# Kernel optimization log

Measured on AMD Instinct MI355X. Metric: run time of the kernel, lower is better.

## Reference

```python
import jax, jax.numpy as jnp
import numpy as np

B, N0, N1, N2 = 4, 50000, 25000, 12500
E0, E1 = 800000, 400000
CIN, CS, COUT = 32, 16, 32
EPS = 1e-5


def _xavier(k, shape):
    scale = (2.0 / (shape[0] + shape[-1])) ** 0.5
    return jax.random.normal(k, shape, jnp.float32) * scale


def setup_inputs() -> dict:
    key = jax.random.key(0)
    ks = jax.random.split(key, 32)
    inp = {
        "X": jax.random.normal(ks[0], (B, N0, CIN), jnp.float32),
        "edge_index0": jax.random.randint(ks[1], (2, E0), 0, N1),
        "edge_weight0": jax.random.uniform(ks[2], (E0,), jnp.float32),
        "res_n_id0": jax.random.randint(ks[3], (N1,), 0, N0),
        "edge_index1": jax.random.randint(ks[4], (2, E1), 0, N2),
        "edge_weight1": jax.random.uniform(ks[5], (E1,), jnp.float32),
        "res_n_id1": jax.random.randint(ks[6], (N2,), 0, N1),
        # conv1 params (in=32 -> out=16, edge_channels=1)
        "Wn1": _xavier(ks[7], (CIN, CS)),
        "We1": _xavier(ks[8], (1, CS)),
        "Q1": _xavier(ks[9], (CS, CS)),
        "K1": _xavier(ks[10], (CS, CS)),
        "Watt1": _xavier(ks[11], (3 * CS, 1)),
        "batt1": jnp.zeros((1,), jnp.float32),
        "Wc1": _xavier(ks[12], (2 * CS, CS)),
        "bc1": jnp.zeros((CS,), jnp.float32),
        # conv2 params (in=16 -> out=32, edge_channels=1)
        "Wn2": _xavier(ks[13], (CS, COUT)),
        "We2": _xavier(ks[14], (1, COUT)),
        "Q2": _xavier(ks[15], (COUT, COUT)),
        "K2": _xavier(ks[16], (COUT, COUT)),
        "Watt2": _xavier(ks[17], (3 * COUT, 1)),
        "batt2": jnp.zeros((1,), jnp.float32),
        "Wc2": _xavier(ks[18], (2 * COUT, COUT)),
        "bc2": jnp.zeros((COUT,), jnp.float32),
    }
    return inp


def egnn_conv(x_src, x_dst, edge_index, edge_feature, num_dst,
              Wn, We, Q, K, Watt, batt, Wc, bc):
    # x_src: [B, Nsrc, Cin], x_dst: [B, Ndst, Cin], edge_feature: [E, 1]
    xs = jnp.matmul(x_src, Wn)        # [B, Nsrc, C]
    xd = jnp.matmul(x_dst, Wn)        # [B, Ndst, C]
    edge_emb = jnp.matmul(edge_feature, We)  # [E, C]

    src, dst = edge_index[0], edge_index[1]
    x_j = xs[:, src]                  # gather [B, E, C]
    x_i = xd[:, dst]                  # gather [B, E, C]

    query = jnp.matmul(x_j, Q)        # [B, E, C]
    key = jnp.matmul(x_i, K)          # [B, E, C]
    ee = jnp.broadcast_to(edge_emb[None], query.shape)  # [B, E, C]
    att_feature = jnp.concatenate([query, key, ee], axis=-1)  # [B, E, 3C]
    att = jax.nn.sigmoid(jnp.matmul(att_feature, Watt) + batt)  # [B, E, 1]
    gate = jax.nn.sigmoid(edge_emb)[None]  # [1, E, C]
    msg = att * x_j * gate            # [B, E, C]

    # scatter-add over destination nodes
    aggr = jnp.zeros((msg.shape[0], num_dst, msg.shape[-1]), msg.dtype)
    aggr = aggr.at[:, dst].add(msg)   # [B, Ndst, C]

    out = jnp.matmul(jnp.concatenate([xd, aggr], axis=-1), Wc) + bc  # [B, Ndst, C]
    mean = jnp.mean(out, axis=(0, 2), keepdims=True)
    var = jnp.var(out, axis=(0, 2), keepdims=True, ddof=1)  # torch var is unbiased
    out = (out - mean) / jnp.sqrt(var + EPS)
    return xd + out


def reference(X, edge_index0, edge_weight0, res_n_id0,
              edge_index1, edge_weight1, res_n_id1,
              Wn1, We1, Q1, K1, Watt1, batt1, Wc1, bc1,
              Wn2, We2, Q2, K2, Watt2, batt2, Wc2, bc2):
    h = egnn_conv(X, X[:, res_n_id0], edge_index0, edge_weight0[:, None], N1,
                  Wn1, We1, Q1, K1, Watt1, batt1, Wc1, bc1)
    h = jax.nn.leaky_relu(h, 0.01)
    h = egnn_conv(h, h[:, res_n_id1], edge_index1, edge_weight1[:, None], N2,
                  Wn2, We2, Q2, K2, Watt2, batt2, Wc2, bc2)
    h = jax.nn.leaky_relu(h, 0.01)
    return h
```

## Files before the change

### kernel.cpp

```cpp
#include <hip/hip_runtime.h>

#define B_ 4
#define N0_ 50000
#define N1_ 25000
#define N2_ 12500
#define E0_ 800000
#define E1_ 400000
#define CIN_ 32
#define CS_ 16
#define COUT_ 32
#define EPS_ 1e-5f
#define CAP_ 80
#define SST1_ 3200
#define SST2_ 1600

__device__ __forceinline__ int slice_of(int d) { return (d >> 2) & 7; }
__device__ __forceinline__ int curix(int d, int sst) {
    return ((d >> 2) & 7) * sst + ((d >> 5) << 2) + (d & 3);
}
__device__ __forceinline__ float sigmoidf_(float x) {
    return __builtin_amdgcn_rcpf(1.0f + __expf(-x));
}

__global__ void prep_kernel(const float* __restrict__ Q1, const float* __restrict__ K1,
                            const float* __restrict__ Watt1,
                            const float* __restrict__ Q2, const float* __restrict__ K2,
                            const float* __restrict__ Watt2,
                            const float* __restrict__ We1, const float* __restrict__ We2,
                            float* __restrict__ qv1, float* __restrict__ kv1,
                            float* __restrict__ qv2, float* __restrict__ kv2,
                            float* __restrict__ se) {
    int t = threadIdx.x;
    if (t < CS_) {
        float q = 0.f, k = 0.f;
        for (int c = 0; c < CS_; ++c) {
            q += Q1[t * CS_ + c] * Watt1[c];
            k += K1[t * CS_ + c] * Watt1[CS_ + c];
        }
        qv1[t] = q; kv1[t] = k;
    }
    if (t < COUT_) {
        float q = 0.f, k = 0.f;
        for (int c = 0; c < COUT_; ++c) {
            q += Q2[t * COUT_ + c] * Watt2[c];
            k += K2[t * COUT_ + c] * Watt2[COUT_ + c];
        }
        qv2[t] = q; kv2[t] = k;
    }
    if (t == 0) {
        float s1 = 0.f, s2 = 0.f;
        for (int c = 0; c < CS_; ++c) s1 += We1[c] * Watt1[2 * CS_ + c];
        for (int c = 0; c < COUT_; ++c) s2 += We2[c] * Watt2[2 * COUT_ + c];
        se[0] = s1; se[1] = s2;
    }
}

__global__ void node_xform1(const float* __restrict__ X, const int* __restrict__ res,
                            const float* __restrict__ Wn,
                            const float* __restrict__ qv, const float* __restrict__ kv,
                            unsigned short* __restrict__ xsb, float* __restrict__ xd_t,
                            float* __restrict__ aj, float* __restrict__ ai) {
    int lane = threadIdx.x & 63;
    int n = blockIdx.x * (blockDim.x >> 6) + (threadIdx.x >> 6);
    if (n >= N1_) return;
    int b = lane >> 4;
    int c = lane & 15;
    int rn = res[n];
    const float4* Xs4 = (const float4*)(X + ((size_t)b * N0_ + n) * CIN_);
    const float4* Xd4 = (const float4*)(X + ((size_t)b * N0_ + rn) * CIN_);
    float s = 0.f, d = 0.f;
#pragma unroll
    for (int k4 = 0; k4 < CIN_ / 4; ++k4) {
        float4 xs4 = Xs4[k4];
        float4 xd4 = Xd4[k4];
        int k = 4 * k4;
        float w0 = Wn[(k + 0) * CS_ + c], w1 = Wn[(k + 1) * CS_ + c];
        float w2 = Wn[(k + 2) * CS_ + c], w3 = Wn[(k + 3) * CS_ + c];
        s += xs4.x * w0 + xs4.y * w1 + xs4.z * w2 + xs4.w * w3;
        d += xd4.x * w0 + xd4.y * w1 + xd4.z * w2 + xd4.w * w3;
    }
    xsb[(size_t)n * 64 + lane] = (unsigned short)((__float_as_uint(s) + 0x8000u) >> 16);
    xd_t[(size_t)n * 64 + lane] = d;
    float p = s * qv[c];
    float q = d * kv[c];
#pragma unroll
    for (int m = 1; m < 16; m <<= 1) {
        p += __shfl_xor(p, m, 16);
        q += __shfl_xor(q, m, 16);
    }
    if (c == 0) {
        aj[n * 4 + b] = p;
        ai[n * 4 + b] = q;
    }
}

template <int SST>
__global__ void scatter_att(const int* __restrict__ ei, const float* __restrict__ ew,
                            int E, const float* __restrict__ aj, const float* __restrict__ ai,
                            const float* __restrict__ sep, const float* __restrict__ batt,
                            int* __restrict__ cur, uint2* __restrict__ buf) {
    int slice = blockIdx.x & 7;
    int chunk = blockIdx.x >> 3;
    int nch = gridDim.x >> 3;
    float se = sep[0], b0 = batt[0];
    for (int e = chunk * 256 + threadIdx.x; e < E; e += nch * 256) {
        int d = ei[E + e];
        if (slice_of(d) != slice) continue;
        int s = ei[e];
        float w = ew[e];
        float4 A = ((const float4*)aj)[s];
        float4 I = ((const float4*)ai)[d];
        float base = fmaf(w, se, b0);
        unsigned q =  __float2uint_rn(sigmoidf_(A.x + I.x + base) * 255.f)
                   | (__float2uint_rn(sigmoidf_(A.y + I.y + base) * 255.f) << 8)
                   | (__float2uint_rn(sigmoidf_(A.z + I.z + base) * 255.f) << 16)
                   | (__float2uint_rn(sigmoidf_(A.w + I.w + base) * 255.f) << 24);
        unsigned wv = (__float_as_uint(w) + 0x8000u) & 0xffff0000u;
        int p = atomicAdd(&cur[curix(d, SST)], 1);
        if (p < CAP_)
            buf[(size_t)d * CAP_ + p] = make_uint2(wv | (unsigned)s, q);
    }
}

__global__ void edge_fused1(const int* __restrict__ cur, const uint2* __restrict__ buf,
                            const unsigned short* __restrict__ xsb,
                            const float* __restrict__ xd_t, const float* __restrict__ We,
                            const float* __restrict__ Wc, const float* __restrict__ bc,
                            float* __restrict__ h_t) {
    int lane = threadIdx.x & 63;
    int n = blockIdx.x * (blockDim.x >> 6) + (threadIdx.x >> 6);
    if (n >= N1_) return;
    int b = lane >> 4;
    int c = lane & 15;
    int sh = 8 * b;
    float wec = We[c];
    float acc = 0.f;
    int cnt = cur[curix(n, SST1_)];
    if (cnt > CAP_) cnt = CAP_;
    const uint2* bp = buf + (size_t)n * CAP_;
    int i = 0;
    for (; i + 4 <= cnt; i += 4) {
        uint2 v0 = bp[i], v1 = bp[i + 1], v2 = bp[i + 2], v3 = bp[i + 3];
        int s0 = v0.x & 0xffff, s1 = v1.x & 0xffff;
        int s2 = v2.x & 0xffff, s3 = v3.x & 0xffff;
        float w0 = __uint_as_float(v0.x & 0xffff0000u);
        float w1 = __uint_as_float(v1.x & 0xffff0000u);
        float w2 = __uint_as_float(v2.x & 0xffff0000u);
        float w3 = __uint_as_float(v3.x & 0xffff0000u);
        float xj0 = __uint_as_float((unsigned)xsb[(size_t)s0 * 64 + lane] << 16);
        float xj1 = __uint_as_float((unsigned)xsb[(size_t)s1 * 64 + lane] << 16);
        float xj2 = __uint_as_float((unsigned)xsb[(size_t)s2 * 64 + lane] << 16);
        float xj3 = __uint_as_float((unsigned)xsb[(size_t)s3 * 64 + lane] << 16);
        float a0 = (float)((v0.y >> sh) & 0xff) * (1.f / 255.f);
        float a1 = (float)((v1.y >> sh) & 0xff) * (1.f / 255.f);
        float a2 = (float)((v2.y >> sh) & 0xff) * (1.f / 255.f);
        float a3 = (float)((v3.y >> sh) & 0xff) * (1.f / 255.f);
        acc += a0 * sigmoidf_(w0 * wec) * xj0;
        acc += a1 * sigmoidf_(w1 * wec) * xj1;
        acc += a2 * sigmoidf_(w2 * wec) * xj2;
        acc += a3 * sigmoidf_(w3 * wec) * xj3;
    }
    for (; i < cnt; ++i) {
        uint2 v0 = bp[i];
        int s0 = v0.x & 0xffff;
        float w0 = __uint_as_float(v0.x & 0xffff0000u);
        float xj0 = __uint_as_float((unsigned)xsb[(size_t)s0 * 64 + lane] << 16);
        float a0 = (float)((v0.y >> sh) & 0xff) * (1.f / 255.f);
        acc += a0 * sigmoidf_(w0 * wec) * xj0;
    }
    float xv = xd_t[(size_t)n * 64 + lane];
    float o = bc[c];
#pragma unroll
    for (int k = 0; k < CS_; ++k) {
        o += __shfl(xv, k, 16) * Wc[k * CS_ + c];
        o += __shfl(acc, k, 16) * Wc[(CS_ + k) * CS_ + c];
    }
    float s = o, sq = o * o;
#pragma unroll
    for (int m = 1; m < 64; m <<= 1) {
        s += __shfl_xor(s, m);
        sq += __shfl_xor(sq, m);
    }
    float mean = s * (1.f / 64.f);
    float var = (sq - 64.f * mean * mean) * (1.f / 63.f);
    float inv = __builtin_amdgcn_rsqf(var + EPS_);
    float v = xv + (o - mean) * inv;
    h_t[(size_t)n * 64 + lane] = v > 0.f ? v : 0.01f * v;
}

__global__ void node_xform2(const float* __restrict__ h_t, const int* __restrict__ res,
                            const float* __restrict__ Wn,
                            const float* __restrict__ qv, const float* __restrict__ kv,
                            unsigned short* __restrict__ xsb, float* __restrict__ xd_t,
                            float* __restrict__ aj, float* __restrict__ ai) {
    int lane = threadIdx.x & 63;
    int n = blockIdx.x * (blockDim.x >> 6) + (threadIdx.x >> 6);
    if (n >= N2_) return;
    int bl = lane >> 5;
    int c = lane & 31;
    int rn = res[n];
    float qc = qv[c], kc = kv[c];
#pragma unroll
    for (int j = 0; j < 2; ++j) {
        int b = bl + 2 * j;
        const float* hs = h_t + (size_t)n * 64 + b * 16;
        const float* hd = h_t + (size_t)rn * 64 + b * 16;
        float s = 0.f, d = 0.f;
#pragma unroll
        for (int k = 0; k < CS_; ++k) {
            float w = Wn[k * COUT_ + c];
            s += hs[k] * w;
            d += hd[k] * w;
        }
        xsb[(size_t)n * 128 + b * 32 + c] = (unsigned short)((__float_as_uint(s) + 0x8000u) >> 16);
        xd_t[(size_t)n * 128 + b * 32 + c] = d;
        float p = s * qc;
        float q = d * kc;
#pragma unroll
        for (int m = 1; m < 32; m <<= 1) {
            p += __shfl_xor(p, m, 32);
            q += __shfl_xor(q, m, 32);
        }
        if (c == 0) {
            aj[n * 4 + b] = p;
            ai[n * 4 + b] = q;
        }
    }
}

__global__ void edge_fused2(const int* __restrict__ cur, const uint2* __restrict__ buf,
                            const unsigned short* __restrict__ xsb,
                            const float* __restrict__ xd_t, const float* __restrict__ We,
                            const float* __restrict__ Wc, const float* __restrict__ bc,
                            float* __restrict__ out) {
    int lane = threadIdx.x & 63;
    int n = blockIdx.x * (blockDim.x >> 6) + (threadIdx.x >> 6);
    if (n >= N2_) return;
    int bl = lane >> 5;
    int c = lane & 31;
    int sh0 = 8 * bl;
    float wec = We[c];
    float acc0 = 0.f, acc1 = 0.f;
    int cnt = cur[curix(n, SST2_)];
    if (cnt > CAP_) cnt = CAP_;
    const uint2* bp = buf + (size_t)n * CAP_;
    int i = 0;
    for (; i + 4 <= cnt; i += 4) {
        uint2 v0 = bp[i], v1 = bp[i + 1], v2 = bp[i + 2], v3 = bp[i + 3];
        int s0 = v0.x & 0xffff, s1 = v1.x & 0xffff;
        int s2 = v2.x & 0xffff, s3 = v3.x & 0xffff;
        float w0 = __uint_as_float(v0.x & 0xffff0000u);
        float w1 = __uint_as_float(v1.x & 0xffff0000u);
        float w2 = __uint_as_float(v2.x & 0xffff0000u);
        float w3 = __uint_as_float(v3.x & 0xffff0000u);
        float xj00 = __uint_as_float((unsigned)xsb[(size_t)s0 * 128 + lane] << 16);
        float xj01 = __uint_as_float((unsigned)xsb[(size_t)s0 * 128 + 64 + lane] << 16);
        float xj10 = __uint_as_float((unsigned)xsb[(size_t)s1 * 128 + lane] << 16);
        float xj11 = __uint_as_float((unsigned)xsb[(size_t)s1 * 128 + 64 + lane] << 16);
        float xj20 = __uint_as_float((unsigned)xsb[(size_t)s2 * 128 + lane] << 16);
        float xj21 = __uint_as_float((unsigned)xsb[(size_t)s2 * 128 + 64 + lane] << 16);
        float xj30 = __uint_as_float((unsigned)xsb[(size_t)s3 * 128 + lane] << 16);
        float xj31 = __uint_as_float((unsigned)xsb[(size_t)s3 * 128 + 64 + lane] << 16);
        float g0 = sigmoidf_(w0 * wec);
        float g1 = sigmoidf_(w1 * wec);
        float g2 = sigmoidf_(w2 * wec);
        float g3 = sigmoidf_(w3 * wec);
        acc0 += (float)((v0.y >> sh0) & 0xff) * (1.f / 255.f) * g0 * xj00;
        acc1 += (float)((v0.y >> (sh0 + 16)) & 0xff) * (1.f / 255.f) * g0 * xj01;
        acc0 += (float)((v1.y >> sh0) & 0xff) * (1.f / 255.f) * g1 * xj10;
        acc1 += (float)((v1.y >> (sh0 + 16)) & 0xff) * (1.f / 255.f) * g1 * xj11;
        acc0 += (float)((v2.y >> sh0) & 0xff) * (1.f / 255.f) * g2 * xj20;
        acc1 += (float)((v2.y >> (sh0 + 16)) & 0xff) * (1.f / 255.f) * g2 * xj21;
        acc0 += (float)((v3.y >> sh0) & 0xff) * (1.f / 255.f) * g3 * xj30;
        acc1 += (float)((v3.y >> (sh0 + 16)) & 0xff) * (1.f / 255.f) * g3 * xj31;
    }
    for (; i < cnt; ++i) {
        uint2 v0 = bp[i];
        int s0 = v0.x & 0xffff;
        float w0 = __uint_as_float(v0.x & 0xffff0000u);
        float xj00 = __uint_as_float((unsigned)xsb[(size_t)s0 * 128 + lane] << 16);
        float xj01 = __uint_as_float((unsigned)xsb[(size_t)s0 * 128 + 64 + lane] << 16);
        float a00 = (float)((v0.y >> sh0) & 0xff) * (1.f / 255.f);
        float a01 = (float)((v0.y >> (sh0 + 16)) & 0xff) * (1.f / 255.f);
        float g0 = sigmoidf_(w0 * wec);
        acc0 += a00 * g0 * xj00;
        acc1 += a01 * g0 * xj01;
    }
    float xv0 = xd_t[(size_t)n * 128 + lane];
    float xv1 = xd_t[(size_t)n * 128 + 64 + lane];
    float o0 = bc[c], o1 = o0;
#pragma unroll
    for (int k = 0; k < COUT_; ++k) {
        float w1 = Wc[k * COUT_ + c];
        float w2 = Wc[(COUT_ + k) * COUT_ + c];
        o0 += __shfl(xv0, k, 32) * w1 + __shfl(acc0, k, 32) * w2;
        o1 += __shfl(xv1, k, 32) * w1 + __shfl(acc1, k, 32) * w2;
    }
    float s = o0 + o1, sq = o0 * o0 + o1 * o1;
#pragma unroll
    for (int m = 1; m < 64; m <<= 1) {
        s += __shfl_xor(s, m);
        sq += __shfl_xor(sq, m);
    }
    float mean = s * (1.f / 128.f);
    float var = (sq - 128.f * mean * mean) * (1.f / 127.f);
    float inv = __builtin_amdgcn_rsqf(var + EPS_);
    float v0 = xv0 + (o0 - mean) * inv;
    float v1 = xv1 + (o1 - mean) * inv;
    out[((size_t)bl * N2_ + n) * COUT_ + c] = v0 > 0.f ? v0 : 0.01f * v0;
    out[((size_t)(bl + 2) * N2_ + n) * COUT_ + c] = v1 > 0.f ? v1 : 0.01f * v1;
}

extern "C" void kernel_launch(void* const* d_in, const int* in_sizes, int n_in,
                              void* d_out, int out_size, void* d_ws, size_t ws_size,
                              hipStream_t stream) {
    (void)in_sizes; (void)n_in; (void)out_size; (void)ws_size;
    const float* X     = (const float*)d_in[0];
    const int*   ei0   = (const int*)d_in[1];
    const float* ew0   = (const float*)d_in[2];
    const int*   rn0   = (const int*)d_in[3];
    const int*   ei1   = (const int*)d_in[4];
    const float* ew1   = (const float*)d_in[5];
    const int*   rn1   = (const int*)d_in[6];
    const float* Wn1   = (const float*)d_in[7];
    const float* We1   = (const float*)d_in[8];
    const float* Q1    = (const float*)d_in[9];
    const float* K1    = (const float*)d_in[10];
    const float* Watt1 = (const float*)d_in[11];
    const float* batt1 = (const float*)d_in[12];
    const float* Wc1   = (const float*)d_in[13];
    const float* bc1   = (const float*)d_in[14];
    const float* Wn2   = (const float*)d_in[15];
    const float* We2   = (const float*)d_in[16];
    const float* Q2    = (const float*)d_in[17];
    const float* K2    = (const float*)d_in[18];
    const float* Watt2 = (const float*)d_in[19];
    const float* batt2 = (const float*)d_in[20];
    const float* Wc2   = (const float*)d_in[21];
    const float* bc2   = (const float*)d_in[22];

    const size_t BUF = (size_t)B_ * N1_ * CS_;
    float* ws  = (float*)d_ws;
    float* S0  = ws;
    float* S1  = S0 + BUF;
    unsigned short* S2 = (unsigned short*)(S1 + BUF);
    float* aj1 = (float*)(S2 + BUF);
    float* ai1 = aj1 + (size_t)N1_ * 4;
    float* aj2 = ai1 + (size_t)N1_ * 4;
    float* ai2 = aj2 + (size_t)N2_ * 4;
    uint2* ebuf = (uint2*)(ai2 + (size_t)N2_ * 4);
    int* cur1 = (int*)(ebuf + (size_t)N1_ * CAP_);
    int* cur2 = cur1 + 8 * SST1_;
    float* qv1 = (float*)(cur2 + 8 * SST2_);
    float* kv1 = qv1 + 16;
    float* qv2 = kv1 + 16;
    float* kv2 = qv2 + 32;
    float* se  = kv2 + 32;

    hipMemsetAsync(cur1, 0, (size_t)(8 * SST1_ + 8 * SST2_) * sizeof(int), stream);
    prep_kernel<<<1, 64, 0, stream>>>(Q1, K1, Watt1, Q2, K2, Watt2, We1, We2,
                                      qv1, kv1, qv2, kv2, se);

    node_xform1<<<(N1_ + 3) / 4, 256, 0, stream>>>(X, rn0, Wn1, qv1, kv1, S2, S0, aj1, ai1);
    scatter_att<SST1_><<<4096, 256, 0, stream>>>(ei0, ew0, E0_, aj1, ai1, se, batt1,
                                                 cur1, ebuf);
    edge_fused1<<<(N1_ + 3) / 4, 256, 0, stream>>>(cur1, ebuf, S2, S0, We1, Wc1, bc1, S0);

    node_xform2<<<(N2_ + 3) / 4, 256, 0, stream>>>(S0, rn1, Wn2, qv2, kv2, S2, S1, aj2, ai2);
    scatter_att<SST2_><<<2048, 256, 0, stream>>>(ei1, ew1, E1_, aj2, ai2, se + 1, batt2,
                                                 cur2, ebuf);
    edge_fused2<<<(N2_ + 3) / 4, 256, 0, stream>>>(cur2, ebuf, S2, S1, We2, Wc2, bc2,
                                                   (float*)d_out);
}
```

Baseline: 190.0 us.

## Pre-pack edge indices and weights, fold memset into prep, unroll gather by 8

A new prep kernel packs each edge's src/dst indices into one 32-bit word and its weight into a bf16 halfword, zeroes the slot counters itself instead of calling a separate memset, and still computes the attention projection vectors. The scatter kernels, which run 8 slice passes over the edge list, now read 6 bytes per edge instead of 12, cutting repeated edge-list traffic. The edge_fused1 gather loop is unrolled to 8 for more loads in flight. The packing pass adds a full read of the edge lists plus extra writes, and the 16-bit packing assumes node ids below 65536.

```diff
diff --git a/kernel.cpp b/kernel.cpp
--- a/kernel.cpp
+++ b/kernel.cpp
@@ -22,36 +22,54 @@
     return __builtin_amdgcn_rcpf(1.0f + __expf(-x));
 }
 
-__global__ void prep_kernel(const float* __restrict__ Q1, const float* __restrict__ K1,
-                            const float* __restrict__ Watt1,
-                            const float* __restrict__ Q2, const float* __restrict__ K2,
-                            const float* __restrict__ Watt2,
-                            const float* __restrict__ We1, const float* __restrict__ We2,
-                            float* __restrict__ qv1, float* __restrict__ kv1,
-                            float* __restrict__ qv2, float* __restrict__ kv2,
-                            float* __restrict__ se) {
-    int t = threadIdx.x;
-    if (t < CS_) {
-        float q = 0.f, k = 0.f;
-        for (int c = 0; c < CS_; ++c) {
-            q += Q1[t * CS_ + c] * Watt1[c];
-            k += K1[t * CS_ + c] * Watt1[CS_ + c];
-        }
-        qv1[t] = q; kv1[t] = k;
-    }
-    if (t < COUT_) {
-        float q = 0.f, k = 0.f;
-        for (int c = 0; c < COUT_; ++c) {
-            q += Q2[t * COUT_ + c] * Watt2[c];
-            k += K2[t * COUT_ + c] * Watt2[COUT_ + c];
-        }
-        qv2[t] = q; kv2[t] = k;
-    }
-    if (t == 0) {
-        float s1 = 0.f, s2 = 0.f;
-        for (int c = 0; c < CS_; ++c) s1 += We1[c] * Watt1[2 * CS_ + c];
-        for (int c = 0; c < COUT_; ++c) s2 += We2[c] * Watt2[2 * COUT_ + c];
-        se[0] = s1; se[1] = s2;
+__global__ void pack_prep(const int* __restrict__ ei0, const float* __restrict__ ew0,
+                          const int* __restrict__ ei1, const float* __restrict__ ew1,
+                          unsigned* __restrict__ pk0, unsigned short* __restrict__ wq0,
+                          unsigned* __restrict__ pk1, unsigned short* __restrict__ wq1,
+                          int* __restrict__ curz, int ztot,
+                          const float* __restrict__ Q1, const float* __restrict__ K1,
+                          const float* __restrict__ Watt1,
+                          const float* __restrict__ Q2, const float* __restrict__ K2,
+                          const float* __restrict__ Watt2,
+                          const float* __restrict__ We1, const float* __restrict__ We2,
+                          float* __restrict__ qv1, float* __restrict__ kv1,
+                          float* __restrict__ qv2, float* __restrict__ kv2,
+                          float* __restrict__ se) {
+    int gid = blockIdx.x * blockDim.x + threadIdx.x;
+    int stride = gridDim.x * blockDim.x;
+    for (int i = gid; i < ztot; i += stride) curz[i] = 0;
+    for (int e = gid; e < E0_; e += stride) {
+        pk0[e] = (unsigned)ei0[e] << 16 | (unsigned)ei0[E0_ + e];
+        wq0[e] = (unsigned short)((__float_as_uint(ew0[e]) + 0x8000u) >> 16);
+    }
+    for (int e = gid; e < E1_; e += stride) {
+        pk1[e] = (unsigned)ei1[e] << 16 | (unsigned)ei1[E1_ + e];
+        wq1[e] = (unsigned short)((__float_as_uint(ew1[e]) + 0x8000u) >> 16);
+    }
+    if (blockIdx.x == 0) {
+        int t = threadIdx.x;
+        if (t < CS_) {
+            float q = 0.f, k = 0.f;
+            for (int c = 0; c < CS_; ++c) {
+                q += Q1[t * CS_ + c] * Watt1[c];
+                k += K1[t * CS_ + c] * Watt1[CS_ + c];
+            }
+            qv1[t] = q; kv1[t] = k;
+        }
+        if (t < COUT_) {
+            float q = 0.f, k = 0.f;
+            for (int c = 0; c < COUT_; ++c) {
+                q += Q2[t * COUT_ + c] * Watt2[c];
+                k += K2[t * COUT_ + c] * Watt2[COUT_ + c];
+            }
+            qv2[t] = q; kv2[t] = k;
+        }
+        if (t == 64) {
+            float s1 = 0.f, s2 = 0.f;
+            for (int c = 0; c < CS_; ++c) s1 += We1[c] * Watt1[2 * CS_ + c];
+            for (int c = 0; c < COUT_; ++c) s2 += We2[c] * Watt2[2 * COUT_ + c];
+            se[0] = s1; se[1] = s2;
+        }
     }
 }
 
@@ -95,7 +113,7 @@
 }
 
 template <int SST>
-__global__ void scatter_att(const int* __restrict__ ei, const float* __restrict__ ew,
+__global__ void scatter_att(const unsigned* __restrict__ pk, const unsigned short* __restrict__ wq,
                             int E, const float* __restrict__ aj, const float* __restrict__ ai,
                             const float* __restrict__ sep, const float* __restrict__ batt,
                             int* __restrict__ cur, uint2* __restrict__ buf) {
@@ -104,10 +122,12 @@
     int nch = gridDim.x >> 3;
     float se = sep[0], b0 = batt[0];
     for (int e = chunk * 256 + threadIdx.x; e < E; e += nch * 256) {
-        int d = ei[E + e];
+        unsigned pv = pk[e];
+        int d = pv & 0xffff;
         if (slice_of(d) != slice) continue;
-        int s = ei[e];
-        float w = ew[e];
+        int s = pv >> 16;
+        unsigned wu = (unsigned)wq[e];
+        float w = __uint_as_float(wu << 16);
         float4 A = ((const float4*)aj)[s];
         float4 I = ((const float4*)ai)[d];
         float base = fmaf(w, se, b0);
@@ -115,10 +135,9 @@
                    | (__float2uint_rn(sigmoidf_(A.y + I.y + base) * 255.f) << 8)
                    | (__float2uint_rn(sigmoidf_(A.z + I.z + base) * 255.f) << 16)
                    | (__float2uint_rn(sigmoidf_(A.w + I.w + base) * 255.f) << 24);
-        unsigned wv = (__float_as_uint(w) + 0x8000u) & 0xffff0000u;
         int p = atomicAdd(&cur[curix(d, SST)], 1);
         if (p < CAP_)
-            buf[(size_t)d * CAP_ + p] = make_uint2(wv | (unsigned)s, q);
+            buf[(size_t)d * CAP_ + p] = make_uint2((wu << 16) | (unsigned)s, q);
     }
 }
 
@@ -139,26 +158,20 @@
     if (cnt > CAP_) cnt = CAP_;
     const uint2* bp = buf + (size_t)n * CAP_;
     int i = 0;
-    for (; i + 4 <= cnt; i += 4) {
-        uint2 v0 = bp[i], v1 = bp[i + 1], v2 = bp[i + 2], v3 = bp[i + 3];
-        int s0 = v0.x & 0xffff, s1 = v1.x & 0xffff;
-        int s2 = v2.x & 0xffff, s3 = v3.x & 0xffff;
-        float w0 = __uint_as_float(v0.x & 0xffff0000u);
-        float w1 = __uint_as_float(v1.x & 0xffff0000u);
-        float w2 = __uint_as_float(v2.x & 0xffff0000u);
-        float w3 = __uint_as_float(v3.x & 0xffff0000u);
-        float xj0 = __uint_as_float((unsigned)xsb[(size_t)s0 * 64 + lane] << 16);
-        float xj1 = __uint_as_float((unsigned)xsb[(size_t)s1 * 64 + lane] << 16);
-        float xj2 = __uint_as_float((unsigned)xsb[(size_t)s2 * 64 + lane] << 16);
-        float xj3 = __uint_as_float((unsigned)xsb[(size_t)s3 * 64 + lane] << 16);
-        float a0 = (float)((v0.y >> sh) & 0xff) * (1.f / 255.f);
-        float a1 = (float)((v1.y >> sh) & 0xff) * (1.f / 255.f);
-        float a2 = (float)((v2.y >> sh) & 0xff) * (1.f / 255.f);
-        float a3 = (float)((v3.y >> sh) & 0xff) * (1.f / 255.f);
-        acc += a0 * sigmoidf_(w0 * wec) * xj0;
-        acc += a1 * sigmoidf_(w1 * wec) * xj1;
-        acc += a2 * sigmoidf_(w2 * wec) * xj2;
-        acc += a3 * sigmoidf_(w3 * wec) * xj3;
+    for (; i + 8 <= cnt; i += 8) {
+        uint2 v[8];
+#pragma unroll
+        for (int j = 0; j < 8; ++j) v[j] = bp[i + j];
+        float xj[8], a[8], g[8];
+#pragma unroll
+        for (int j = 0; j < 8; ++j) {
+            int sj = v[j].x & 0xffff;
+            xj[j] = __uint_as_float((unsigned)xsb[(size_t)sj * 64 + lane] << 16);
+            a[j] = (float)((v[j].y >> sh) & 0xff) * (1.f / 255.f);
+            g[j] = sigmoidf_(__uint_as_float(v[j].x & 0xffff0000u) * wec);
+        }
+#pragma unroll
+        for (int j = 0; j < 8; ++j) acc += a[j] * g[j] * xj[j];
     }
     for (; i < cnt; ++i) {
         uint2 v0 = bp[i];
@@ -351,23 +364,29 @@
     uint2* ebuf = (uint2*)(ai2 + (size_t)N2_ * 4);
     int* cur1 = (int*)(ebuf + (size_t)N1_ * CAP_);
     int* cur2 = cur1 + 8 * SST1_;
-    float* qv1 = (float*)(cur2 + 8 * SST2_);
+    unsigned* pk0 = (unsigned*)(cur2 + 8 * SST2_);
+    unsigned* pk1 = pk0 + E0_;
+    unsigned short* wq0 = (unsigned short*)(pk1 + E1_);
+    unsigned short* wq1 = wq0 + E0_;
+    float* qv1 = (float*)(wq1 + E1_);
     float* kv1 = qv1 + 16;
     float* qv2 = kv1 + 16;
     float* kv2 = qv2 + 32;
     float* se  = kv2 + 32;
 
-    hipMemsetAsync(cur1, 0, (size_t)(8 * SST1_ + 8 * SST2_) * sizeof(int), stream);
-    prep_kernel<<<1, 64, 0, stream>>>(Q1, K1, Watt1, Q2, K2, Watt2, We1, We2,
-                                      qv1, kv1, qv2, kv2, se);
+    const int ztot = 8 * SST1_ + 8 * SST2_;
+    pack_prep<<<1024, 256, 0, stream>>>(ei0, ew0, ei1, ew1, pk0, wq0, pk1, wq1,
+                                        cur1, ztot,
+                                        Q1, K1, Watt1, Q2, K2, Watt2, We1, We2,
+                                        qv1, kv1, qv2, kv2, se);
 
     node_xform1<<<(N1_ + 3) / 4, 256, 0, stream>>>(X, rn0, Wn1, qv1, kv1, S2, S0, aj1, ai1);
-    scatter_att<SST1_><<<4096, 256, 0, stream>>>(ei0, ew0, E0_, aj1, ai1, se, batt1,
+    scatter_att<SST1_><<<4096, 256, 0, stream>>>(pk0, wq0, E0_, aj1, ai1, se, batt1,
                                                  cur1, ebuf);
     edge_fused1<<<(N1_ + 3) / 4, 256, 0, stream>>>(cur1, ebuf, S2, S0, We1, Wc1, bc1, S0);
 
     node_xform2<<<(N2_ + 3) / 4, 256, 0, stream>>>(S0, rn1, Wn2, qv2, kv2, S2, S1, aj2, ai2);
-    scatter_att<SST2_><<<2048, 256, 0, stream>>>(ei1, ew1, E1_, aj2, ai2, se + 1, batt2,
+    scatter_att<SST2_><<<2048, 256, 0, stream>>>(pk1, wq1, E1_, aj2, ai2, se + 1, batt2,
                                                  cur2, ebuf);
     edge_fused2<<<(N2_ + 3) / 4, 256, 0, stream>>>(cur2, ebuf, S2, S1, We2, Wc2, bc2,
                                                    (float*)d_out);
```

New measurement: 183.9 us. 3.2% less time.
